# Kernel tuning notes

Hardware: AMD Instinct MI355X
Metric: run time of the kernel (lower is better)

## Reference

```python
import jax, jax.numpy as jnp
import numpy as np

D_MODEL = 1024
D_STATE = 16
EXPAND = 2
D_INNER = D_MODEL * EXPAND          # 2048
DT_RANK = (D_MODEL + 15) // 16      # 64 (auto)
BATCH = 2
SEQ = 1024


def setup_inputs() -> dict:
    key = jax.random.key(0)
    ks = jax.random.split(key, 8)
    def nrm(k, shape, scale):
        return jax.random.normal(k, shape, dtype=jnp.float32) * scale
    x = jax.random.normal(ks[0], (BATCH, SEQ, D_MODEL), dtype=jnp.float32)
    W_in = nrm(ks[1], (D_MODEL, 2 * D_INNER), D_MODEL ** -0.5)
    W_conv = nrm(ks[2], (D_INNER, 3), 3 ** -0.5)           # depthwise kernel, taps [t-2,t-1,t]
    W_x = nrm(ks[3], (D_INNER, DT_RANK + 2 * D_STATE), D_INNER ** -0.5)
    W_dt = nrm(ks[4], (DT_RANK, D_INNER), DT_RANK ** -0.5)
    b_dt = nrm(ks[5], (D_INNER,), 0.1)
    # A_log init exactly as in the torch module: log(arange(1..d_state)) per channel
    A_log = jnp.log(jnp.tile(jnp.arange(1, D_STATE + 1, dtype=jnp.float32), (D_INNER, 1)))
    D_param = jnp.ones((D_INNER,), dtype=jnp.float32)
    W_out = nrm(ks[6], (D_INNER, D_MODEL), D_INNER ** -0.5)
    return {"x": x, "W_in": W_in, "W_conv": W_conv, "W_x": W_x,
            "W_dt": W_dt, "b_dt": b_dt, "A_log": A_log, "D_param": D_param,
            "W_out": W_out}


def _s6_forward(x, W_in, W_conv, W_x, W_dt, b_dt, A_log, D_param, W_out):
    B, L, _ = x.shape
    # input projection -> (u, res)
    u, res = jnp.split(x @ W_in, 2, axis=-1)           # each [B, L, d_inner]
    # depthwise causal conv, kernel=3, left pad 2 (matches Conv1d(pad=2)[..., :L])
    up = jnp.pad(u, ((0, 0), (2, 0), (0, 0)))
    u = (up[:, :L] * W_conv[:, 0]
         + up[:, 1:L + 1] * W_conv[:, 1]
         + up[:, 2:L + 2] * W_conv[:, 2])
    u = jax.nn.silu(u)
    # input-dependent SSM params
    x_dbl = u @ W_x                                     # [B, L, dt_rank + 2*d_state]
    dt, Bm, Cm = jnp.split(x_dbl, [DT_RANK, DT_RANK + D_STATE], axis=-1)
    delta = jax.nn.softplus(dt @ W_dt + b_dt)           # [B, L, d_inner]
    A = -jnp.exp(A_log)                                 # [d_inner, d_state]
    deltaA = jnp.exp(jnp.einsum('bld,dn->bldn', delta, A))     # [B, L, D, N]
    deltaB_u = jnp.einsum('bld,bln->bldn', delta * u, Bm)      # [B, L, D, N]
    # sequential selective scan over L via lax.scan
    def step(h, inp):
        dA, dbu, c = inp                # dA,dbu: [B,D,N], c: [B,N]
        h = dA * h + dbu
        y = jnp.einsum('bdn,bn->bd', h, c)
        return h, y
    h0 = jnp.zeros((B, D_INNER, D_STATE), dtype=u.dtype)
    _, ys = jax.lax.scan(step, h0, (jnp.moveaxis(deltaA, 1, 0),
                                    jnp.moveaxis(deltaB_u, 1, 0),
                                    jnp.moveaxis(Cm, 1, 0)))
    y = jnp.moveaxis(ys, 0, 1)                          # [B, L, d_inner]
    y = y + u * D_param
    y = y * jax.nn.silu(res)
    return y @ W_out                                    # [B, L, d_model]


def reference(x, W_in, W_conv, W_x, W_dt, b_dt, A_log, D_param, W_out):
    return _s6_forward(x, W_in, W_conv, W_x, W_dt, b_dt, A_log, D_param, W_out)
```

## Files before the change

kernel.cpp:

```cpp
#include <hip/hip_runtime.h>
#include <math.h>
#include <stdint.h>

#define BATCH 2
#define SEQ   1024
#define DM    1024
#define DI    2048
#define DS    16
#define DTR   64
#define ROWS  (BATCH*SEQ)
#define CH    32
#define NCH   (SEQ/CH)
#define NSPLIT 16
#define G4SPLIT 4

typedef unsigned short u16;
typedef __bf16 bf16x8 __attribute__((ext_vector_type(8)));
typedef float  f32x4  __attribute__((ext_vector_type(4)));
typedef short  short8 __attribute__((ext_vector_type(8)));

__device__ __forceinline__ float bf2f(u16 v) {
    return __uint_as_float(((unsigned)v) << 16);
}
__device__ __forceinline__ u16 f2bf(float f) {
    unsigned u = __float_as_uint(f);
    return (u16)((u + 0x7FFFu + ((u >> 16) & 1u)) >> 16);
}
__device__ __forceinline__ float softplus_f(float v) {
    return fmaxf(v, 0.f) + __logf(1.f + __expf(-fabsf(v)));
}
__device__ __forceinline__ float silu_f(float v) {
    return v / (1.f + __expf(-v));
}

__device__ __forceinline__ void gload16(const void* g, const void* l) {
    __builtin_amdgcn_global_load_lds(
        (const __attribute__((address_space(1))) unsigned int*)(uintptr_t)g,
        (__attribute__((address_space(3))) unsigned int*)(uintptr_t)l,
        16, 0, 0);
}

template<int EPI, typename TOUT>
__global__ __launch_bounds__(256) void gemm_bf16(
    const u16* __restrict__ A,
    const u16* __restrict__ BT,
    TOUT* __restrict__ C, u16* __restrict__ C2,
    int ldc, int N, int Ksplit, long long zCstride,
    const float* __restrict__ bias)
{
    __shared__ u16 As[2][128 * 32];
    __shared__ u16 Bs[2][128 * 32];

    const int K = (int)gridDim.z * Ksplit;
    int tid  = threadIdx.x;
    int lane = tid & 63, wid = tid >> 6;
    int wr = wid >> 1, wc = wid & 1;
    int row0 = blockIdx.y * 128, col0 = blockIdx.x * 128;
    int kbeg = blockIdx.z * Ksplit;
    const int niter = Ksplit >> 5;

    int sRow = wid * 32 + (lane >> 2);
    int sOff = (lane & 3) * 8;

    const u16* Abase = A  + (size_t)(row0 + sRow) * K + sOff;
    const u16* Bbase = BT + (size_t)(col0 + sRow) * K + sOff;

    int frow = lane & 15;
    int fk   = (lane >> 4) * 8;

    f32x4 acc[4][4] = {};

    #pragma unroll
    for (int c = 0; c < 2; ++c) {
        gload16(Abase + (size_t)c * 16 * K + kbeg, As[0] + (wid * 32 + c * 16) * 32);
        gload16(Bbase + (size_t)c * 16 * K + kbeg, Bs[0] + (wid * 32 + c * 16) * 32);
    }

    for (int i = 0; i < niter; ++i) {
        __syncthreads();
        int cur = i & 1;
        if (i + 1 < niter) {
            int kn = kbeg + (i + 1) * 32;
            int nxt = cur ^ 1;
            #pragma unroll
            for (int c = 0; c < 2; ++c) {
                gload16(Abase + (size_t)c * 16 * K + kn, As[nxt] + (wid * 32 + c * 16) * 32);
                gload16(Bbase + (size_t)c * 16 * K + kn, Bs[nxt] + (wid * 32 + c * 16) * 32);
            }
        }
        bf16x8 af[4], bfr[4];
        #pragma unroll
        for (int m = 0; m < 4; ++m)
            af[m] = *(const bf16x8*)(As[cur] + (wr * 64 + m * 16 + frow) * 32 + fk);
        #pragma unroll
        for (int n = 0; n < 4; ++n)
            bfr[n] = *(const bf16x8*)(Bs[cur] + (wc * 64 + n * 16 + frow) * 32 + fk);
        #pragma unroll
        for (int m = 0; m < 4; ++m)
            #pragma unroll
            for (int n = 0; n < 4; ++n)
                acc[m][n] = __builtin_amdgcn_mfma_f32_16x16x32_bf16(
                    af[m], bfr[n], acc[m][n], 0, 0, 0);
    }

    int orow = row0 + wr * 64 + (lane >> 4) * 4;
    int ocol = col0 + wc * 64 + (lane & 15);

    if (EPI == 1) {
        bool isres = (col0 >= 2048);
        #pragma unroll
        for (int m = 0; m < 4; ++m)
            #pragma unroll
            for (int n = 0; n < 4; ++n) {
                int colb = ocol + n * 16 - (isres ? 2048 : 0);
                #pragma unroll
                for (int r = 0; r < 4; ++r) {
                    float v = acc[m][n][r];
                    size_t o = (size_t)(orow + m * 16 + r) * 2048 + colb;
                    if (isres) C2[o] = f2bf(silu_f(v));
                    else       ((u16*)C)[o] = f2bf(v);
                }
            }
    } else if (EPI == 2) {
        #pragma unroll
        for (int m = 0; m < 4; ++m)
            #pragma unroll
            for (int n = 0; n < 4; ++n) {
                int colb = ocol + n * 16;
                float bv = bias[colb];
                #pragma unroll
                for (int r = 0; r < 4; ++r) {
                    float v = softplus_f(acc[m][n][r] + bv);
                    ((u16*)C)[(size_t)(orow + m * 16 + r) * ldc + colb] = f2bf(v);
                }
            }
    } else {
        size_t zoff = (size_t)blockIdx.z * (size_t)zCstride;
        #pragma unroll
        for (int m = 0; m < 4; ++m)
            #pragma unroll
            for (int n = 0; n < 4; ++n) {
                int colb = ocol + n * 16;
                if (colb < N) {
                    #pragma unroll
                    for (int r = 0; r < 4; ++r) {
                        float v = acc[m][n][r];
                        size_t o = zoff + (size_t)(orow + m * 16 + r) * ldc + colb;
                        if constexpr (sizeof(TOUT) == 2) C[o] = (TOUT)f2bf(v);
                        else                             C[o] = (TOUT)v;
                    }
                }
            }
    }
}

__global__ __launch_bounds__(256) void tcast_kernel(
    const float* __restrict__ in, u16* __restrict__ outp,
    int K, int N, int Npad)
{
    __shared__ float tile[32][33];
    int tx = threadIdx.x & 31;
    int ty = threadIdx.x >> 5;
    int k0 = blockIdx.y * 32, n0 = blockIdx.x * 32;
    #pragma unroll
    for (int i = 0; i < 4; ++i) {
        int k = k0 + ty + i * 8, n = n0 + tx;
        tile[ty + i * 8][tx] = (k < K && n < N) ? in[(size_t)k * N + n] : 0.f;
    }
    __syncthreads();
    #pragma unroll
    for (int i = 0; i < 4; ++i) {
        int n = n0 + ty + i * 8, k = k0 + tx;
        if (n < Npad && k < K)
            outp[(size_t)n * K + k] = f2bf(tile[tx][ty + i * 8]);
    }
}

__global__ __launch_bounds__(256) void cast_kernel(
    const float* __restrict__ in, u16* __restrict__ outp, int n)
{
    int i = (blockIdx.x * 256 + threadIdx.x) * 4;
    if (i < n) {
        float4 v = *(const float4*)(in + i);
        outp[i + 0] = f2bf(v.x); outp[i + 1] = f2bf(v.y);
        outp[i + 2] = f2bf(v.z); outp[i + 3] = f2bf(v.w);
    }
}

__global__ __launch_bounds__(256) void reduce_split_kernel(
    const float* __restrict__ part, float* __restrict__ xdbl,
    u16* __restrict__ dtbf)
{
    int i = blockIdx.x * 256 + threadIdx.x;
    if (i < ROWS * 96) {
        float s = 0.f;
        #pragma unroll
        for (int z = 0; z < NSPLIT; ++z) s += part[(size_t)z * ROWS * 96 + i];
        xdbl[i] = s;
        int row = i / 96, col = i - row * 96;
        if (col < 64) dtbf[row * 64 + col] = f2bf(s);
    }
}

__global__ __launch_bounds__(256) void reduce4_kernel(
    const float* __restrict__ part, float* __restrict__ outp)
{
    int i = (blockIdx.x * 256 + threadIdx.x) * 4;
    const size_t S = (size_t)ROWS * 1024;
    float4 a = *(const float4*)(part + i);
    float4 b = *(const float4*)(part + S + i);
    float4 c = *(const float4*)(part + 2 * S + i);
    float4 d = *(const float4*)(part + 3 * S + i);
    float4 o;
    o.x = a.x + b.x + c.x + d.x;
    o.y = a.y + b.y + c.y + d.y;
    o.z = a.z + b.z + c.z + d.z;
    o.w = a.w + b.w + c.w + d.w;
    *(float4*)(outp + i) = o;
}

__global__ __launch_bounds__(256) void conv_silu_kernel(
    const u16* __restrict__ upre,
    const float* __restrict__ Wc,
    u16* __restrict__ u)
{
    int gt = blockIdx.x * 256 + threadIdx.x;
    int d0 = (gt * 8) & (DI - 1);
    int r  = (gt * 8) >> 11;
    int l  = r & (SEQ - 1);
    const u16* rowp = upre + (size_t)r * DI + d0;
    short8 cur = *(const short8*)rowp;
    short8 p1 = {}, p2 = {};
    if (l >= 1) p1 = *(const short8*)(rowp - DI);
    if (l >= 2) p2 = *(const short8*)(rowp - 2 * DI);
    short8 o;
    #pragma unroll
    for (int j = 0; j < 8; ++j) {
        float w0 = Wc[(d0 + j) * 3 + 0];
        float w1 = Wc[(d0 + j) * 3 + 1];
        float w2 = Wc[(d0 + j) * 3 + 2];
        float v = w2 * bf2f((u16)cur[j]) + w1 * bf2f((u16)p1[j]) + w0 * bf2f((u16)p2[j]);
        o[j] = (short)f2bf(silu_f(v));
    }
    *(short8*)(u + (size_t)r * DI + d0) = o;
}

__global__ __launch_bounds__(256) void scan_chunk_kernel(
    const u16*  __restrict__ dvbf,
    const u16*  __restrict__ u,
    const float* __restrict__ xdbl,
    const float* __restrict__ A_log,
    float* __restrict__ P,
    float* __restrict__ Q)
{
    int gtid = blockIdx.x * 256 + threadIdx.x;
    int nq = gtid & 3;
    int d  = (gtid >> 2) & (DI - 1);
    int rc = gtid >> 13;
    int chunk = rc & (NCH - 1);
    int b = rc >> 5;

    float4 a4 = *(const float4*)(A_log + (size_t)d * DS + nq * 4);
    float Av[4] = {-__expf(a4.x), -__expf(a4.y), -__expf(a4.z), -__expf(a4.w)};
    float h[4] = {};
    float dsum = 0.f;

    int l0 = chunk * CH;
    const u16* drow = dvbf + ((size_t)b * SEQ + l0) * DI + d;
    const u16* urow = u    + ((size_t)b * SEQ + l0) * DI + d;
    const float* xrow = xdbl + ((size_t)b * SEQ + l0) * 96 + 64 + nq * 4;

    #pragma unroll 4
    for (int l = 0; l < CH; ++l) {
        float dv = bf2f(drow[(size_t)l * DI]);
        float du = dv * bf2f(urow[(size_t)l * DI]);
        dsum += dv;
        float4 b4 = *(const float4*)(xrow + l * 96);
        h[0] = __expf(dv * Av[0]) * h[0] + du * b4.x;
        h[1] = __expf(dv * Av[1]) * h[1] + du * b4.y;
        h[2] = __expf(dv * Av[2]) * h[2] + du * b4.z;
        h[3] = __expf(dv * Av[3]) * h[3] + du * b4.w;
    }
    size_t off = ((size_t)(b * NCH + chunk) * DI + d) * DS + nq * 4;
    float4 p4 = {__expf(dsum * Av[0]), __expf(dsum * Av[1]),
                 __expf(dsum * Av[2]), __expf(dsum * Av[3])};
    *(float4*)(P + off) = p4;
    *(float4*)(Q + off) = make_float4(h[0], h[1], h[2], h[3]);
}

__global__ __launch_bounds__(256) void scan_combine_kernel(
    const float* __restrict__ P,
    float* __restrict__ Q)
{
    int idx = blockIdx.x * 256 + threadIdx.x;
    int nd = idx & (DI * DS - 1);
    int b = idx >> 15;
    float h = 0.f;
    for (int c = 0; c < NCH; ++c) {
        size_t off = (size_t)(b * NCH + c) * DI * DS + nd;
        float p = P[off], q = Q[off];
        Q[off] = h;
        h = p * h + q;
    }
}

__global__ __launch_bounds__(256) void scan_final_kernel(
    const u16*  __restrict__ dvbf,
    const u16*  __restrict__ u,
    const float* __restrict__ xdbl,
    const float* __restrict__ A_log,
    const float* __restrict__ hin,
    const u16*  __restrict__ resbf,
    const float* __restrict__ Dp,
    u16* __restrict__ yf)
{
    int gtid = blockIdx.x * 256 + threadIdx.x;
    int nq = gtid & 3;
    int d  = (gtid >> 2) & (DI - 1);
    int rc = gtid >> 13;
    int chunk = rc & (NCH - 1);
    int b = rc >> 5;

    float4 a4 = *(const float4*)(A_log + (size_t)d * DS + nq * 4);
    float Av[4] = {-__expf(a4.x), -__expf(a4.y), -__expf(a4.z), -__expf(a4.w)};
    size_t off = ((size_t)(b * NCH + chunk) * DI + d) * DS + nq * 4;
    float4 h4 = *(const float4*)(hin + off);
    float h[4] = {h4.x, h4.y, h4.z, h4.w};
    float Dd = Dp[d];

    int l0 = chunk * CH;
    const u16* drow = dvbf + ((size_t)b * SEQ + l0) * DI + d;
    const u16* urow = u    + ((size_t)b * SEQ + l0) * DI + d;
    const float* xrow = xdbl + ((size_t)b * SEQ + l0) * 96 + 64 + nq * 4;
    const u16* rrow = resbf + ((size_t)b * SEQ + l0) * DI + d;
    u16* yrow = yf + ((size_t)b * SEQ + l0) * DI + d;

    #pragma unroll 4
    for (int l = 0; l < CH; ++l) {
        float dv = bf2f(drow[(size_t)l * DI]);
        float uv = bf2f(urow[(size_t)l * DI]);
        float du = dv * uv;
        float4 b4 = *(const float4*)(xrow + l * 96);
        float4 c4 = *(const float4*)(xrow + l * 96 + 16);
        h[0] = __expf(dv * Av[0]) * h[0] + du * b4.x;
        h[1] = __expf(dv * Av[1]) * h[1] + du * b4.y;
        h[2] = __expf(dv * Av[2]) * h[2] + du * b4.z;
        h[3] = __expf(dv * Av[3]) * h[3] + du * b4.w;
        float y = h[0] * c4.x + h[1] * c4.y + h[2] * c4.z + h[3] * c4.w;
        y += __shfl_xor(y, 1);
        y += __shfl_xor(y, 2);
        if (nq == 0) {
            float v = (y + uv * Dd) * bf2f(rrow[(size_t)l * DI]);
            yrow[(size_t)l * DI] = f2bf(v);
        }
    }
}

extern "C" void kernel_launch(void* const* d_in, const int* in_sizes, int n_in,
                              void* d_out, int out_size, void* d_ws, size_t ws_size,
                              hipStream_t stream) {
    const float* x       = (const float*)d_in[0];
    const float* W_in    = (const float*)d_in[1];
    const float* W_conv  = (const float*)d_in[2];
    const float* W_x     = (const float*)d_in[3];
    const float* W_dt    = (const float*)d_in[4];
    const float* b_dt    = (const float*)d_in[5];
    const float* A_log   = (const float*)d_in[6];
    const float* D_param = (const float*)d_in[7];
    const float* W_out   = (const float*)d_in[8];
    float* out = (float*)d_out;

    float* buf0  = (float*)d_ws;
    float* D16   = buf0 + (size_t)ROWS * 4096;
    float* Qbuf  = D16 + (size_t)ROWS * DI;
    float* R1    = Qbuf + (size_t)BATCH * NCH * DI * DS;
    float* R2    = R1 + 2 * 1024 * 1024;
    float* xdbl  = R2 + 1024 * 1024;
    u16*  u_bf   = (u16*)(xdbl + (size_t)ROWS * 96);
    u16*  WxT    = (u16*)(u_bf + (size_t)ROWS * DI);

    u16* u_pre_bf = (u16*)D16;
    u16* res_bf   = (u16*)D16 + (size_t)ROWS * DI;
    u16* dv_bf    = (u16*)D16;
    u16* WinT  = (u16*)R1;
    u16* WdtT  = (u16*)R1;
    u16* dtbf  = (u16*)R1 + 2048 * 64;
    float* P   = R1;
    u16* yf    = (u16*)R1;
    float* Xpart  = buf0;
    float* G4part = buf0;
    u16* xbf   = (u16*)R2;
    u16* WoutT = (u16*)R2;

    dim3 blk(256);

    tcast_kernel<<<dim3(4096/32, 1024/32), blk, 0, stream>>>(W_in, WinT, 1024, 4096, 4096);
    cast_kernel<<<(ROWS * DM / 4 + 255) / 256, blk, 0, stream>>>(x, xbf, ROWS * DM);

    gemm_bf16<1, u16><<<dim3(4096/128, ROWS/128, 1), blk, 0, stream>>>(
        xbf, WinT, u_pre_bf, res_bf, 2048, 4096, 1024, 0, nullptr);

    tcast_kernel<<<dim3(1024/32, 2048/32), blk, 0, stream>>>(W_out, WoutT, 2048, 1024, 1024);
    tcast_kernel<<<dim3(2048/32, 64/32), blk, 0, stream>>>(W_dt, WdtT, 64, 2048, 2048);
    tcast_kernel<<<dim3(128/32, 2048/32), blk, 0, stream>>>(W_x, WxT, 2048, 96, 128);

    conv_silu_kernel<<<(ROWS * DI / 8) / 256, blk, 0, stream>>>(u_pre_bf, W_conv, u_bf);

    gemm_bf16<0, float><<<dim3(1, ROWS/128, NSPLIT), blk, 0, stream>>>(
        u_bf, WxT, Xpart, nullptr, 96, 96, DI / NSPLIT, (long long)ROWS * 96, nullptr);
    reduce_split_kernel<<<(ROWS * 96 + 255) / 256, blk, 0, stream>>>(Xpart, xdbl, dtbf);

    gemm_bf16<2, u16><<<dim3(DI/128, ROWS/128, 1), blk, 0, stream>>>(
        dtbf, WdtT, dv_bf, nullptr, DI, DI, DTR, 0, b_dt);

    scan_chunk_kernel<<<(BATCH * NCH * DI * 4) / 256, blk, 0, stream>>>(
        dv_bf, u_bf, xdbl, A_log, P, Qbuf);
    scan_combine_kernel<<<(BATCH * DI * DS) / 256, blk, 0, stream>>>(P, Qbuf);
    scan_final_kernel<<<(BATCH * NCH * DI * 4) / 256, blk, 0, stream>>>(
        dv_bf, u_bf, xdbl, A_log, Qbuf, res_bf, D_param, yf);

    gemm_bf16<0, float><<<dim3(1024/128, ROWS/128, G4SPLIT), blk, 0, stream>>>(
        yf, WoutT, G4part, nullptr, 1024, 1024, 2048 / G4SPLIT, (long long)ROWS * 1024, nullptr);
    reduce4_kernel<<<(ROWS * 1024 / 4) / 256, blk, 0, stream>>>(G4part, out);
}
```

Measured before the change: 158.5 us.

## Deepen GEMM K-tile to 64 with XOR-swizzled LDS and batch scan loads

```diff
diff --git a/kernel.cpp b/kernel.cpp
--- a/kernel.cpp
+++ b/kernel.cpp
@@ -48,8 +48,8 @@
     int ldc, int N, int Ksplit, long long zCstride,
     const float* __restrict__ bias)
 {
-    __shared__ u16 As[2][128 * 32];
-    __shared__ u16 Bs[2][128 * 32];
+    __shared__ u16 As[2][128 * 64];
+    __shared__ u16 Bs[2][128 * 64];
 
     const int K = (int)gridDim.z * Ksplit;
     int tid  = threadIdx.x;
@@ -57,51 +57,62 @@
     int wr = wid >> 1, wc = wid & 1;
     int row0 = blockIdx.y * 128, col0 = blockIdx.x * 128;
     int kbeg = blockIdx.z * Ksplit;
-    const int niter = Ksplit >> 5;
-
-    int sRow = wid * 32 + (lane >> 2);
-    int sOff = (lane & 3) * 8;
-
-    const u16* Abase = A  + (size_t)(row0 + sRow) * K + sOff;
-    const u16* Bbase = BT + (size_t)(col0 + sRow) * K + sOff;
+    const int niter = Ksplit >> 6;
+
+    int sRow = wid * 32 + (lane >> 3);
+    int sCol = (((lane & 7) ^ ((lane >> 3) & 7))) * 8;
+
+    const u16* Abase = A  + (size_t)(row0 + sRow) * K + sCol;
+    const u16* Bbase = BT + (size_t)(col0 + sRow) * K + sCol;
 
     int frow = lane & 15;
-    int fk   = (lane >> 4) * 8;
+    int s0   = lane >> 4;
+    int r7   = lane & 7;
 
     f32x4 acc[4][4] = {};
 
-    #pragma unroll
-    for (int c = 0; c < 2; ++c) {
-        gload16(Abase + (size_t)c * 16 * K + kbeg, As[0] + (wid * 32 + c * 16) * 32);
-        gload16(Bbase + (size_t)c * 16 * K + kbeg, Bs[0] + (wid * 32 + c * 16) * 32);
-    }
+#define STAGE(buf, kk)                                                          \
+    do {                                                                        \
+        _Pragma("unroll")                                                       \
+        for (int c = 0; c < 4; ++c) {                                           \
+            gload16(Abase + (size_t)c * 8 * K + (kk),                           \
+                    As[buf] + (wid * 32 + c * 8) * 64);                         \
+            gload16(Bbase + (size_t)c * 8 * K + (kk),                           \
+                    Bs[buf] + (wid * 32 + c * 8) * 64);                         \
+        }                                                                       \
+    } while (0)
+
+    STAGE(0, kbeg);
 
     for (int i = 0; i < niter; ++i) {
         __syncthreads();
         int cur = i & 1;
-        if (i + 1 < niter) {
-            int kn = kbeg + (i + 1) * 32;
-            int nxt = cur ^ 1;
-            #pragma unroll
-            for (int c = 0; c < 2; ++c) {
-                gload16(Abase + (size_t)c * 16 * K + kn, As[nxt] + (wid * 32 + c * 16) * 32);
-                gload16(Bbase + (size_t)c * 16 * K + kn, Bs[nxt] + (wid * 32 + c * 16) * 32);
-            }
+        if (i + 1 < niter) STAGE(cur ^ 1, kbeg + (i + 1) * 64);
+
+        #pragma unroll
+        for (int kk = 0; kk < 2; ++kk) {
+            bf16x8 af[4], bfr[4];
+            #pragma unroll
+            for (int m = 0; m < 4; ++m) {
+                int row = wr * 64 + m * 16 + frow;
+                int off = row * 64 + (((kk * 4 + s0) ^ r7) * 8);
+                af[m] = *(const bf16x8*)(As[cur] + off);
+            }
+            #pragma unroll
+            for (int n = 0; n < 4; ++n) {
+                int row = wc * 64 + n * 16 + frow;
+                int off = row * 64 + (((kk * 4 + s0) ^ r7) * 8);
+                bfr[n] = *(const bf16x8*)(Bs[cur] + off);
+            }
+            #pragma unroll
+            for (int m = 0; m < 4; ++m)
+                #pragma unroll
+                for (int n = 0; n < 4; ++n)
+                    acc[m][n] = __builtin_amdgcn_mfma_f32_16x16x32_bf16(
+                        af[m], bfr[n], acc[m][n], 0, 0, 0);
         }
-        bf16x8 af[4], bfr[4];
-        #pragma unroll
-        for (int m = 0; m < 4; ++m)
-            af[m] = *(const bf16x8*)(As[cur] + (wr * 64 + m * 16 + frow) * 32 + fk);
-        #pragma unroll
-        for (int n = 0; n < 4; ++n)
-            bfr[n] = *(const bf16x8*)(Bs[cur] + (wc * 64 + n * 16 + frow) * 32 + fk);
-        #pragma unroll
-        for (int m = 0; m < 4; ++m)
-            #pragma unroll
-            for (int n = 0; n < 4; ++n)
-                acc[m][n] = __builtin_amdgcn_mfma_f32_16x16x32_bf16(
-                    af[m], bfr[n], acc[m][n], 0, 0, 0);
-    }
+    }
+#undef STAGE
 
     int orow = row0 + wr * 64 + (lane >> 4) * 4;
     int ocol = col0 + wc * 64 + (lane & 15);
@@ -270,16 +281,27 @@
     const u16* urow = u    + ((size_t)b * SEQ + l0) * DI + d;
     const float* xrow = xdbl + ((size_t)b * SEQ + l0) * 96 + 64 + nq * 4;
 
-    #pragma unroll 4
-    for (int l = 0; l < CH; ++l) {
-        float dv = bf2f(drow[(size_t)l * DI]);
-        float du = dv * bf2f(urow[(size_t)l * DI]);
-        dsum += dv;
-        float4 b4 = *(const float4*)(xrow + l * 96);
-        h[0] = __expf(dv * Av[0]) * h[0] + du * b4.x;
-        h[1] = __expf(dv * Av[1]) * h[1] + du * b4.y;
-        h[2] = __expf(dv * Av[2]) * h[2] + du * b4.z;
-        h[3] = __expf(dv * Av[3]) * h[3] + du * b4.w;
+    #pragma unroll
+    for (int half = 0; half < 2; ++half) {
+        float dvv[16], uvv[16];
+        #pragma unroll
+        for (int j = 0; j < 16; ++j) {
+            int l = half * 16 + j;
+            dvv[j] = bf2f(drow[(size_t)l * DI]);
+            uvv[j] = bf2f(urow[(size_t)l * DI]);
+        }
+        #pragma unroll
+        for (int j = 0; j < 16; ++j) {
+            int l = half * 16 + j;
+            float dv = dvv[j];
+            float du = dv * uvv[j];
+            dsum += dv;
+            float4 b4 = *(const float4*)(xrow + l * 96);
+            h[0] = __expf(dv * Av[0]) * h[0] + du * b4.x;
+            h[1] = __expf(dv * Av[1]) * h[1] + du * b4.y;
+            h[2] = __expf(dv * Av[2]) * h[2] + du * b4.z;
+            h[3] = __expf(dv * Av[3]) * h[3] + du * b4.w;
+        }
     }
     size_t off = ((size_t)(b * NCH + chunk) * DI + d) * DS + nq * 4;
     float4 p4 = {__expf(dsum * Av[0]), __expf(dsum * Av[1]),
@@ -335,23 +357,34 @@
     const u16* rrow = resbf + ((size_t)b * SEQ + l0) * DI + d;
     u16* yrow = yf + ((size_t)b * SEQ + l0) * DI + d;
 
-    #pragma unroll 4
-    for (int l = 0; l < CH; ++l) {
-        float dv = bf2f(drow[(size_t)l * DI]);
-        float uv = bf2f(urow[(size_t)l * DI]);
-        float du = dv * uv;
-        float4 b4 = *(const float4*)(xrow + l * 96);
-        float4 c4 = *(const float4*)(xrow + l * 96 + 16);
-        h[0] = __expf(dv * Av[0]) * h[0] + du * b4.x;
-        h[1] = __expf(dv * Av[1]) * h[1] + du * b4.y;
-        h[2] = __expf(dv * Av[2]) * h[2] + du * b4.z;
-        h[3] = __expf(dv * Av[3]) * h[3] + du * b4.w;
-        float y = h[0] * c4.x + h[1] * c4.y + h[2] * c4.z + h[3] * c4.w;
-        y += __shfl_xor(y, 1);
-        y += __shfl_xor(y, 2);
-        if (nq == 0) {
-            float v = (y + uv * Dd) * bf2f(rrow[(size_t)l * DI]);
-            yrow[(size_t)l * DI] = f2bf(v);
+    #pragma unroll
+    for (int half = 0; half < 2; ++half) {
+        float dvv[16], uvv[16];
+        #pragma unroll
+        for (int j = 0; j < 16; ++j) {
+            int l = half * 16 + j;
+            dvv[j] = bf2f(drow[(size_t)l * DI]);
+            uvv[j] = bf2f(urow[(size_t)l * DI]);
+        }
+        #pragma unroll
+        for (int j = 0; j < 16; ++j) {
+            int l = half * 16 + j;
+            float dv = dvv[j];
+            float uv = uvv[j];
+            float du = dv * uv;
+            float4 b4 = *(const float4*)(xrow + l * 96);
+            float4 c4 = *(const float4*)(xrow + l * 96 + 16);
+            h[0] = __expf(dv * Av[0]) * h[0] + du * b4.x;
+            h[1] = __expf(dv * Av[1]) * h[1] + du * b4.y;
+            h[2] = __expf(dv * Av[2]) * h[2] + du * b4.z;
+            h[3] = __expf(dv * Av[3]) * h[3] + du * b4.w;
+            float y = h[0] * c4.x + h[1] * c4.y + h[2] * c4.z + h[3] * c4.w;
+            y += __shfl_xor(y, 1);
+            y += __shfl_xor(y, 2);
+            if (nq == 0) {
+                float v = (y + uv * Dd) * bf2f(rrow[(size_t)l * DI]);
+                yrow[(size_t)l * DI] = f2bf(v);
+            }
         }
     }
 }
```

Result: slower. 164.3 us (+3.6%).
